# Kernel tuning notes

Measured on AMD Instinct MI355X. Metric: run time of the kernel, lower is better.

The kernel has to match this reference:

```python
import jax, jax.numpy as jnp
import numpy as np

N_NODES, N_EDGES, F_IN = 8192, 32768, 16
N_SUB, N_GRAPH = 512, 32
EDGE_DIM, HID = 5, 128
DIMS = [(16, 32), (32, 64), (64, 64)]  # (M_in, M_out) per NNConv layer


def _segment_mean(x, seg, n):
    s = jax.ops.segment_sum(x, seg, num_segments=n)
    c = jax.ops.segment_sum(jnp.ones((x.shape[0], 1), x.dtype), seg, num_segments=n)
    return s / jnp.maximum(c, 1.0)


def _nnconv(x, src, dst, eattr, W1, b1, W2, b2, root, bias):
    # edge MLP -> per-edge weight matrix theta: [E, M_in, M_out]
    h = jax.nn.relu(eattr @ W1 + b1)
    theta = (h @ W2 + b2).reshape(-1, x.shape[1], root.shape[1])
    msg = jnp.einsum('ei,eio->eo', x[src], theta)          # gather + per-edge matvec
    agg = jax.ops.segment_sum(msg, dst, num_segments=x.shape[0])  # scatter-add (aggr='add')
    return agg + x @ root + bias


def setup_inputs() -> dict:
    key = jax.random.key(0)
    ks = jax.random.split(key, 32)
    inp = {}
    inp['x'] = jax.random.normal(ks[0], (N_NODES, F_IN), jnp.float32)
    inp['edge_index'] = jax.random.randint(ks[1], (2, N_EDGES), 0, N_NODES)
    inp['edge_attr'] = jax.random.uniform(ks[2], (N_EDGES, EDGE_DIM), jnp.float32)
    inp['node_to_subgraph'] = jnp.sort(jax.random.randint(ks[3], (N_NODES,), 0, N_SUB))
    inp['subgraph_to_graph'] = jnp.sort(jax.random.randint(ks[4], (N_SUB,), 0, N_GRAPH))
    i = 5
    for l, (ci, co) in enumerate(DIMS):
        inp[f'W1_{l}'] = jax.random.normal(ks[i], (EDGE_DIM, HID), jnp.float32) * 0.1
        inp[f'b1_{l}'] = jnp.zeros((HID,), jnp.float32)
        inp[f'W2_{l}'] = jax.random.normal(ks[i + 1], (HID, ci * co), jnp.float32) * 0.05
        inp[f'b2_{l}'] = jnp.zeros((ci * co,), jnp.float32)
        inp[f'root_{l}'] = jax.random.normal(ks[i + 2], (ci, co), jnp.float32) * 0.1
        inp[f'bias_{l}'] = jnp.zeros((co,), jnp.float32)
        i += 3
    inp['fc1_w'] = jax.random.normal(ks[i], (64, 32), jnp.float32) * 0.1
    inp['fc1_b'] = jnp.zeros((32,), jnp.float32)
    inp['fc2_w'] = jax.random.normal(ks[i + 1], (32, 16), jnp.float32) * 0.1
    inp['fc2_b'] = jnp.zeros((16,), jnp.float32)
    inp['fc3_w'] = jax.random.normal(ks[i + 2], (16, 1), jnp.float32) * 0.1
    inp['fc3_b'] = jnp.zeros((1,), jnp.float32)
    return inp


def reference(x, edge_index, edge_attr, node_to_subgraph, subgraph_to_graph,
              W1_0, b1_0, W2_0, b2_0, root_0, bias_0,
              W1_1, b1_1, W2_1, b2_1, root_1, bias_1,
              W1_2, b1_2, W2_2, b2_2, root_2, bias_2,
              fc1_w, fc1_b, fc2_w, fc2_b, fc3_w, fc3_b):
    src, dst = edge_index[0], edge_index[1]
    layers = [(W1_0, b1_0, W2_0, b2_0, root_0, bias_0),
              (W1_1, b1_1, W2_1, b2_1, root_1, bias_1),
              (W1_2, b1_2, W2_2, b2_2, root_2, bias_2)]
    h = x
    for (W1, b1, W2, b2, root, bias) in layers:
        h = jax.nn.elu(_nnconv(h, src, dst, edge_attr, W1, b1, W2, b2, root, bias))
    h = _segment_mean(h, node_to_subgraph, N_SUB)      # global_mean_pool over subgraphs
    h = _segment_mean(h, subgraph_to_graph, N_GRAPH)   # global_mean_pool over graphs
    h = jax.nn.elu(h @ fc1_w + fc1_b)
    h = jax.nn.elu(h @ fc2_w + fc2_b)
    return (h @ fc3_w + fc3_b).reshape(-1)
```

## Files before the change

### kernel.cpp

```cpp
#include <hip/hip_runtime.h>

#define E_EDGES 32768
#define NN 8192
#define HID 128

typedef _Float16 half8 __attribute__((ext_vector_type(8)));
typedef _Float16 half4 __attribute__((ext_vector_type(4)));
typedef float f32x4 __attribute__((ext_vector_type(4)));

__device__ __forceinline__ void prep_one(int idx, int l2ci, int l2co,
                                         const float* __restrict__ W2,
                                         const float* __restrict__ b2,
                                         _Float16* __restrict__ out) {
  int CI = 1 << l2ci, CO = 1 << l2co;
  int Kmain = CI << 7;
  int j = idx & 7;
  int n = (idx >> 3) & (CO - 1);
  int kg = idx >> (3 + l2co);
  int k = kg * 8 + j;
  float v = 0.f;
  if (k < Kmain) {
    int hh = k >> l2ci, i = k & (CI - 1);
    v = W2[((hh << l2ci) + i) * CO + n];
  } else if (k < Kmain + CI) {
    v = b2[(k - Kmain) * CO + n];
  }
  out[idx] = (_Float16)v;
}

#define ZTOT (8192 * 32 + 8192 * 64 + 8192 * 64 + 512 * 64 + 512)
#define PREP0 (2176 * 32)
#define PREP1 (4224 * 64)
#define PREP2 (8320 * 64)

__global__ void prep_k(float* __restrict__ zr,
                       const float* __restrict__ W2a, const float* __restrict__ b2a, _Float16* __restrict__ oa,
                       const float* __restrict__ W2b, const float* __restrict__ b2b, _Float16* __restrict__ ob,
                       const float* __restrict__ W2c, const float* __restrict__ b2c, _Float16* __restrict__ oc) {
  int idx = blockIdx.x * 256 + threadIdx.x;
  if (idx < ZTOT) { zr[idx] = 0.f; return; }
  idx -= ZTOT;
  if (idx < PREP0) prep_one(idx, 4, 5, W2a, b2a, oa);
  else if (idx < PREP0 + PREP1) prep_one(idx - PREP0, 5, 6, W2b, b2b, ob);
  else if (idx < PREP0 + PREP1 + PREP2) prep_one(idx - PREP0 - PREP1, 6, 6, W2c, b2c, oc);
}

template <int CI, int CO>
__launch_bounds__(256, 2)
__global__ void msg_mfma_k(const float* __restrict__ xcur, const int* __restrict__ src,
                           const int* __restrict__ dst, const float* __restrict__ eattr,
                           const float* __restrict__ W1, const float* __restrict__ b1,
                           const _Float16* __restrict__ Bsw, float* __restrict__ agg) {
  constexpr int ME = 256;
  constexpr int L2CI = (CI == 64) ? 6 : ((CI == 32) ? 5 : 4);
  constexpr int XSTR = CI + 8;
  constexpr int FC = CO / 16;
  constexpr int C4 = CI / 4;
  constexpr int L2C4 = L2CI - 2;
  constexpr int NV = (CI == 64) ? 2 : 1;
  constexpr int HS = 40;
  constexpr int CW = CI / 4;
  constexpr int RR = CW / 4;

  __shared__ _Float16 he_t[ME * HS];
  __shared__ _Float16 xs_s[ME * XSTR];
  __shared__ float ea_s[ME * 5];
  __shared__ float W1s[5 * 32];
  __shared__ float b1s[32];
  __shared__ int src_s[ME];
  __shared__ int dst_s[ME];

  int t = threadIdx.x;
  int e0 = blockIdx.x * ME;
  int y = blockIdx.y;
  int hbeg = y * 32;

  for (int j = t; j < ME * 5; j += 256) ea_s[j] = eattr[e0 * 5 + j];
  if (t < 5 * 32) W1s[t] = W1[(t >> 5) * HID + hbeg + (t & 31)];
  if (t < 32) b1s[t] = b1[hbeg + t];
  src_s[t] = src[e0 + t];
  dst_s[t] = dst[e0 + t];
  __syncthreads();

  for (int j = t; j < 32 * ME; j += 256) {
    int hl = j >> 8, e = j & (ME - 1);
    float v = b1s[hl];
#pragma unroll
    for (int d = 0; d < 5; ++d) v += ea_s[e * 5 + d] * W1s[d * 32 + hl];
    he_t[e * HS + hl] = (_Float16)fmaxf(v, 0.f);
  }
  for (int j = t; j < ME * C4; j += 256) {
    int e = j >> L2C4, i4 = j & (C4 - 1);
    float4 v = ((const float4*)xcur)[src_s[e] * C4 + i4];
    half4 hq = {(_Float16)v.x, (_Float16)v.y, (_Float16)v.z, (_Float16)v.w};
    *(half4*)&xs_s[e * XSTR + i4 * 4] = hq;
  }
  __syncthreads();

  int lane = t & 63;
  int w = t >> 6;
  int quad = lane >> 4, l15 = lane & 15;

  half8 xreg[4][NV];
#pragma unroll
  for (int fr = 0; fr < 4; ++fr)
#pragma unroll
    for (int v = 0; v < NV; ++v)
      xreg[fr][v] = *(const half8*)&xs_s[(w * 64 + fr * 16 + l15) * XSTR +
                                         ((quad * 8 + v * 32) & (CI - 1))];

  int cbeg = y * CI;
  int ctail_end = cbeg + CI + ((y == 3) ? 4 : 0);

  const half8* bsw8 = (const half8*)Bsw;
  int ib = quad * CO + l15;

  f32x4 acc[4][FC];
#pragma unroll
  for (int fr = 0; fr < 4; ++fr)
#pragma unroll
    for (int fc = 0; fc < FC; ++fc)
#pragma unroll
      for (int r = 0; r < 4; ++r) acc[fr][fc][r] = 0.f;

  half8 breg[4][FC];
#pragma unroll
  for (int j = 0; j < 4; ++j)
#pragma unroll
    for (int fc = 0; fc < FC; ++fc)
      breg[j][fc] = bsw8[(cbeg + j) * 4 * CO + ib + fc * 16];

  for (int win = 0; win < 4; ++win) {
    half8 hreg[4];
#pragma unroll
    for (int fr = 0; fr < 4; ++fr)
      hreg[fr] = *(const half8*)&he_t[(w * 64 + fr * 16 + l15) * HS + win * 8];
#pragma unroll
    for (int rr = 0; rr < RR; ++rr) {
#pragma unroll
      for (int j = 0; j < 4; ++j) {
        int cl = win * CW + rr * 4 + j;
        int c = cbeg + cl;
        constexpr int PAR = (CI == 64) ? 1 : 0;
        int vi = PAR ? (cl & 1) : 0;
        half8 a[4];
#pragma unroll
        for (int fr = 0; fr < 4; ++fr) {
          _Float16 hv;
          if (CI == 16)      hv = (quad & 2) ? hreg[fr][2 * j + 1] : hreg[fr][2 * j];
          else if (CI == 32) hv = hreg[fr][rr * 4 + j];
          else               hv = hreg[fr][(rr * 4 + j) >> 1];
          half8 hb = {hv, hv, hv, hv, hv, hv, hv, hv};
          a[fr] = xreg[fr][vi] * hb;
        }
#pragma unroll
        for (int fc = 0; fc < FC; ++fc) {
#pragma unroll
          for (int fr = 0; fr < 4; ++fr)
            acc[fr][fc] = __builtin_amdgcn_mfma_f32_16x16x32_f16(a[fr], breg[cl & 3][fc], acc[fr][fc], 0, 0, 0);
        }
        int cn = c + 4;
        if (cn >= ctail_end) cn = ctail_end - 1;
#pragma unroll
        for (int fc = 0; fc < FC; ++fc)
          breg[cl & 3][fc] = bsw8[cn * 4 * CO + ib + fc * 16];
      }
    }
  }

  if (y == 3) {
#pragma unroll
    for (int j = 0; j < 4; ++j) {
      int cl = CI + j;
      constexpr int PAR = (CI == 64) ? 1 : 0;
      int vi = PAR ? (cl & 1) : 0;
#pragma unroll
      for (int fc = 0; fc < FC; ++fc) {
#pragma unroll
        for (int fr = 0; fr < 4; ++fr)
          acc[fr][fc] = __builtin_amdgcn_mfma_f32_16x16x32_f16(xreg[fr][vi], breg[cl & 3][fc], acc[fr][fc], 0, 0, 0);
      }
    }
  }

#pragma unroll
  for (int fr = 0; fr < 4; ++fr)
#pragma unroll
    for (int r = 0; r < 4; ++r) {
      int el = w * 64 + fr * 16 + quad * 4 + r;
      int d = dst_s[el];
      float* base = agg + (size_t)d * CO + l15;
#pragma unroll
      for (int fc = 0; fc < FC; ++fc)
        atomicAdd(base + fc * 16, acc[fr][fc][r]);
    }
}

template <int CI, int CO, bool POOL, bool CNT>
__global__ void fin_k(const float* __restrict__ xcur, const float* __restrict__ root,
                      const float* __restrict__ bias, const float* __restrict__ agg,
                      const int* __restrict__ n2s, int* __restrict__ cnt_sub,
                      float* __restrict__ ssum, float* __restrict__ xnext) {
  constexpr int NB = 256 / CO;
  __shared__ float xs[NB * CI];
  int t = threadIdx.x;
  int n0 = blockIdx.x * NB;
  for (int j = t; j < NB * CI; j += 256) xs[j] = xcur[n0 * CI + j];
  __syncthreads();
  int nl = t / CO, o = t & (CO - 1);
  int n = n0 + nl;
  float a = bias[o] + agg[n * CO + o];
#pragma unroll
  for (int i = 0; i < CI; ++i) a += xs[nl * CI + i] * root[i * CO + o];
  float r = a > 0.f ? a : expm1f(a);
  if (CNT && o == 0) atomicAdd(&cnt_sub[n2s[n]], 1);
  if (POOL) atomicAdd(&ssum[(n2s[n] << 6) + o], r);
  else xnext[n * CO + o] = r;
}

__device__ __forceinline__ int lbound(const int* __restrict__ a, int n, int v) {
  int lo = 0, hi = n;
  while (lo < hi) { int m = (lo + hi) >> 1; if (a[m] < v) lo = m + 1; else hi = m; }
  return lo;
}

__global__ void head_k(const float* __restrict__ ssum, const int* __restrict__ cnt_sub,
                       const int* __restrict__ s2g,
                       const float* __restrict__ w1, const float* __restrict__ b1,
                       const float* __restrict__ w2, const float* __restrict__ b2,
                       const float* __restrict__ w3, const float* __restrict__ b3,
                       float* __restrict__ out) {
  int g = blockIdx.x;
  int t = threadIdx.x;
  __shared__ float m[64], s1[32], s2[16];
  int slo = lbound(s2g, 512, g);
  int shi = lbound(s2g, 512, g + 1);
  float acc = 0.f;
  for (int s = slo; s < shi; ++s)
    acc += ssum[(s << 6) + t] / fmaxf((float)cnt_sub[s], 1.f);
  m[t] = acc / fmaxf((float)(shi - slo), 1.f);
  __syncthreads();
  if (t < 32) {
    float a = b1[t];
    for (int i = 0; i < 64; ++i) a += m[i] * w1[i * 32 + t];
    s1[t] = a > 0.f ? a : expm1f(a);
  }
  __syncthreads();
  if (t < 16) {
    float a = b2[t];
    for (int i = 0; i < 32; ++i) a += s1[i] * w2[i * 16 + t];
    s2[t] = a > 0.f ? a : expm1f(a);
  }
  __syncthreads();
  if (t == 0) {
    float a = b3[0];
    for (int i = 0; i < 16; ++i) a += s2[i] * w3[i];
    out[g] = a;
  }
}

extern "C" void kernel_launch(void* const* d_in, const int* in_sizes, int n_in,
                              void* d_out, int out_size, void* d_ws, size_t ws_size,
                              hipStream_t stream) {
  (void)in_sizes; (void)n_in; (void)out_size; (void)ws_size;
  const float* x0 = (const float*)d_in[0];
  const int* ei = (const int*)d_in[1];
  const float* ea = (const float*)d_in[2];
  const int* n2s = (const int*)d_in[3];
  const int* s2g = (const int*)d_in[4];
  const float* W1_[3] = {(const float*)d_in[5], (const float*)d_in[11], (const float*)d_in[17]};
  const float* b1_[3] = {(const float*)d_in[6], (const float*)d_in[12], (const float*)d_in[18]};
  const float* W2_[3] = {(const float*)d_in[7], (const float*)d_in[13], (const float*)d_in[19]};
  const float* b2_[3] = {(const float*)d_in[8], (const float*)d_in[14], (const float*)d_in[20]};
  const float* rt_[3] = {(const float*)d_in[9], (const float*)d_in[15], (const float*)d_in[21]};
  const float* bs_[3] = {(const float*)d_in[10], (const float*)d_in[16], (const float*)d_in[22]};
  const float* fc1w = (const float*)d_in[23]; const float* fc1b = (const float*)d_in[24];
  const float* fc2w = (const float*)d_in[25]; const float* fc2b = (const float*)d_in[26];
  const float* fc3w = (const float*)d_in[27]; const float* fc3b = (const float*)d_in[28];
  float* out = (float*)d_out;

  const int* srcp = ei;
  const int* dstp = ei + E_EDGES;

  char* wsb = (char*)d_ws;
  size_t off = 0;
  auto alloc = [&](size_t bytes) {
    void* p = wsb + off;
    off += (bytes + 255) & ~(size_t)255;
    return p;
  };
  _Float16* Bsw0 = (_Float16*)alloc((size_t)PREP0 * 2);
  _Float16* Bsw1 = (_Float16*)alloc((size_t)PREP1 * 2);
  _Float16* Bsw2 = (_Float16*)alloc((size_t)PREP2 * 2);
  float* agg1 = (float*)alloc((size_t)NN * 32 * 4);
  float* agg2 = (float*)alloc((size_t)NN * 64 * 4);
  float* agg3 = (float*)alloc((size_t)NN * 64 * 4);
  float* ssum = (float*)alloc((size_t)512 * 64 * 4);
  int* cnt_sub = (int*)alloc((size_t)512 * 4);
  float* x1 = (float*)alloc((size_t)NN * 32 * 4);
  float* x2 = (float*)alloc((size_t)NN * 64 * 4);

  const int preptot = ZTOT + PREP0 + PREP1 + PREP2;
  prep_k<<<(preptot + 255) / 256, 256, 0, stream>>>(agg1, W2_[0], b2_[0], Bsw0,
                                                    W2_[1], b2_[1], Bsw1,
                                                    W2_[2], b2_[2], Bsw2);

  dim3 mg(E_EDGES / 256, 4);
  msg_mfma_k<16, 32><<<mg, 256, 0, stream>>>(x0, srcp, dstp, ea, W1_[0], b1_[0], Bsw0, agg1);
  fin_k<16, 32, false, true><<<NN / 8, 256, 0, stream>>>(x0, rt_[0], bs_[0], agg1, n2s, cnt_sub, ssum, x1);
  msg_mfma_k<32, 64><<<mg, 256, 0, stream>>>(x1, srcp, dstp, ea, W1_[1], b1_[1], Bsw1, agg2);
  fin_k<32, 64, false, false><<<NN / 4, 256, 0, stream>>>(x1, rt_[1], bs_[1], agg2, n2s, cnt_sub, ssum, x2);
  msg_mfma_k<64, 64><<<mg, 256, 0, stream>>>(x2, srcp, dstp, ea, W1_[2], b1_[2], Bsw2, agg3);
  fin_k<64, 64, true, false><<<NN / 4, 256, 0, stream>>>(x2, rt_[2], bs_[2], agg3, n2s, cnt_sub, ssum, nullptr);

  head_k<<<32, 64, 0, stream>>>(ssum, cnt_sub, s2g, fc1w, fc1b, fc2w, fc2b, fc3w, fc3b, out);
}
```

Measured before the change: 282.6 us.

## Halve edge tile per block and shrink register buffers for higher occupancy

The edge tile per block drops from 256 to 128 edges, so each wave now handles 32 edges (2 fragments instead of 4). The B-operand register ring shrinks from 4 to 2 entries with a prefetch distance of 2, and launch bounds are raised to 4 blocks per CU. Together these cut register and LDS pressure and double the grid, aiming for better latency hiding and more parallelism. The cost is less reuse of each B load across edges (twice as many B global loads overall), a shorter prefetch distance, and a non-unrolled inner loop.

```diff
diff --git a/kernel.cpp b/kernel.cpp
--- a/kernel.cpp
+++ b/kernel.cpp
@@ -46,12 +46,12 @@
 }
 
 template <int CI, int CO>
-__launch_bounds__(256, 2)
+__launch_bounds__(256, 4)
 __global__ void msg_mfma_k(const float* __restrict__ xcur, const int* __restrict__ src,
                            const int* __restrict__ dst, const float* __restrict__ eattr,
                            const float* __restrict__ W1, const float* __restrict__ b1,
                            const _Float16* __restrict__ Bsw, float* __restrict__ agg) {
-  constexpr int ME = 256;
+  constexpr int ME = 128;
   constexpr int L2CI = (CI == 64) ? 6 : ((CI == 32) ? 5 : 4);
   constexpr int XSTR = CI + 8;
   constexpr int FC = CO / 16;
@@ -60,7 +60,7 @@
   constexpr int NV = (CI == 64) ? 2 : 1;
   constexpr int HS = 40;
   constexpr int CW = CI / 4;
-  constexpr int RR = CW / 4;
+  constexpr int NP = CW / 2;
 
   __shared__ _Float16 he_t[ME * HS];
   __shared__ _Float16 xs_s[ME * XSTR];
@@ -78,12 +78,11 @@
   for (int j = t; j < ME * 5; j += 256) ea_s[j] = eattr[e0 * 5 + j];
   if (t < 5 * 32) W1s[t] = W1[(t >> 5) * HID + hbeg + (t & 31)];
   if (t < 32) b1s[t] = b1[hbeg + t];
-  src_s[t] = src[e0 + t];
-  dst_s[t] = dst[e0 + t];
+  if (t < ME) { src_s[t] = src[e0 + t]; dst_s[t] = dst[e0 + t]; }
   __syncthreads();
 
   for (int j = t; j < 32 * ME; j += 256) {
-    int hl = j >> 8, e = j & (ME - 1);
+    int hl = j >> 7, e = j & (ME - 1);
     float v = b1s[hl];
 #pragma unroll
     for (int d = 0; d < 5; ++d) v += ea_s[e * 5 + d] * W1s[d * 32 + hl];
@@ -100,70 +99,68 @@
   int lane = t & 63;
   int w = t >> 6;
   int quad = lane >> 4, l15 = lane & 15;
-
-  half8 xreg[4][NV];
-#pragma unroll
-  for (int fr = 0; fr < 4; ++fr)
+  int hsel = (quad >> 1) & 1;
+
+  half8 xreg[2][NV];
+#pragma unroll
+  for (int fr = 0; fr < 2; ++fr)
 #pragma unroll
     for (int v = 0; v < NV; ++v)
-      xreg[fr][v] = *(const half8*)&xs_s[(w * 64 + fr * 16 + l15) * XSTR +
+      xreg[fr][v] = *(const half8*)&xs_s[(w * 32 + fr * 16 + l15) * XSTR +
                                          ((quad * 8 + v * 32) & (CI - 1))];
 
   int cbeg = y * CI;
-  int ctail_end = cbeg + CI + ((y == 3) ? 4 : 0);
+  int TC = CI + ((y == 3) ? 4 : 0);
 
   const half8* bsw8 = (const half8*)Bsw;
   int ib = quad * CO + l15;
 
-  f32x4 acc[4][FC];
-#pragma unroll
-  for (int fr = 0; fr < 4; ++fr)
+  f32x4 acc[2][FC];
+#pragma unroll
+  for (int fr = 0; fr < 2; ++fr)
 #pragma unroll
     for (int fc = 0; fc < FC; ++fc)
 #pragma unroll
       for (int r = 0; r < 4; ++r) acc[fr][fc][r] = 0.f;
 
-  half8 breg[4][FC];
-#pragma unroll
-  for (int j = 0; j < 4; ++j)
+  half8 breg[2][FC];
+#pragma unroll
+  for (int p = 0; p < 2; ++p)
 #pragma unroll
     for (int fc = 0; fc < FC; ++fc)
-      breg[j][fc] = bsw8[(cbeg + j) * 4 * CO + ib + fc * 16];
+      breg[p][fc] = bsw8[(cbeg + p) * 4 * CO + ib + fc * 16];
 
   for (int win = 0; win < 4; ++win) {
-    half8 hreg[4];
-#pragma unroll
-    for (int fr = 0; fr < 4; ++fr)
-      hreg[fr] = *(const half8*)&he_t[(w * 64 + fr * 16 + l15) * HS + win * 8];
-#pragma unroll
-    for (int rr = 0; rr < RR; ++rr) {
-#pragma unroll
-      for (int j = 0; j < 4; ++j) {
-        int cl = win * CW + rr * 4 + j;
-        int c = cbeg + cl;
-        constexpr int PAR = (CI == 64) ? 1 : 0;
-        int vi = PAR ? (cl & 1) : 0;
-        half8 a[4];
-#pragma unroll
-        for (int fr = 0; fr < 4; ++fr) {
+    half8 hreg[2];
+#pragma unroll
+    for (int fr = 0; fr < 2; ++fr)
+      hreg[fr] = *(const half8*)&he_t[(w * 32 + fr * 16 + l15) * HS + win * 8];
+    for (int cl2 = 0; cl2 < NP; ++cl2) {
+#pragma unroll
+      for (int p = 0; p < 2; ++p) {
+        int cl = win * CW + cl2 * 2 + p;
+        int vi = (CI == 64) ? p : 0;
+        half8 a[2];
+#pragma unroll
+        for (int fr = 0; fr < 2; ++fr) {
           _Float16 hv;
-          if (CI == 16)      hv = (quad & 2) ? hreg[fr][2 * j + 1] : hreg[fr][2 * j];
-          else if (CI == 32) hv = hreg[fr][rr * 4 + j];
-          else               hv = hreg[fr][(rr * 4 + j) >> 1];
+          if (CI == 16)      hv = hreg[fr][2 * (cl2 * 2 + p) + hsel];
+          else if (CI == 32) hv = hreg[fr][cl2 * 2 + p];
+          else               hv = hreg[fr][cl2];
           half8 hb = {hv, hv, hv, hv, hv, hv, hv, hv};
           a[fr] = xreg[fr][vi] * hb;
         }
 #pragma unroll
         for (int fc = 0; fc < FC; ++fc) {
 #pragma unroll
-          for (int fr = 0; fr < 4; ++fr)
-            acc[fr][fc] = __builtin_amdgcn_mfma_f32_16x16x32_f16(a[fr], breg[cl & 3][fc], acc[fr][fc], 0, 0, 0);
+          for (int fr = 0; fr < 2; ++fr)
+            acc[fr][fc] = __builtin_amdgcn_mfma_f32_16x16x32_f16(a[fr], breg[p][fc], acc[fr][fc], 0, 0, 0);
         }
-        int cn = c + 4;
-        if (cn >= ctail_end) cn = ctail_end - 1;
+        int cn = cl + 2;
+        if (cn >= TC) cn = TC - 1;
 #pragma unroll
         for (int fc = 0; fc < FC; ++fc)
-          breg[cl & 3][fc] = bsw8[cn * 4 * CO + ib + fc * 16];
+          breg[p][fc] = bsw8[(cbeg + cn) * 4 * CO + ib + fc * 16];
       }
     }
   }
@@ -172,22 +169,27 @@
 #pragma unroll
     for (int j = 0; j < 4; ++j) {
       int cl = CI + j;
-      constexpr int PAR = (CI == 64) ? 1 : 0;
-      int vi = PAR ? (cl & 1) : 0;
+      int p = j & 1;
+      int vi = (CI == 64) ? p : 0;
 #pragma unroll
       for (int fc = 0; fc < FC; ++fc) {
 #pragma unroll
-        for (int fr = 0; fr < 4; ++fr)
-          acc[fr][fc] = __builtin_amdgcn_mfma_f32_16x16x32_f16(xreg[fr][vi], breg[cl & 3][fc], acc[fr][fc], 0, 0, 0);
+        for (int fr = 0; fr < 2; ++fr)
+          acc[fr][fc] = __builtin_amdgcn_mfma_f32_16x16x32_f16(xreg[fr][vi], breg[p][fc], acc[fr][fc], 0, 0, 0);
       }
+      int cn = cl + 2;
+      if (cn >= TC) cn = TC - 1;
+#pragma unroll
+      for (int fc = 0; fc < FC; ++fc)
+        breg[p][fc] = bsw8[(cbeg + cn) * 4 * CO + ib + fc * 16];
     }
   }
 
 #pragma unroll
-  for (int fr = 0; fr < 4; ++fr)
+  for (int fr = 0; fr < 2; ++fr)
 #pragma unroll
     for (int r = 0; r < 4; ++r) {
-      int el = w * 64 + fr * 16 + quad * 4 + r;
+      int el = w * 32 + fr * 16 + quad * 4 + r;
       int d = dst_s[el];
       float* base = agg + (size_t)d * CO + l15;
 #pragma unroll
@@ -305,7 +307,7 @@
                                                     W2_[1], b2_[1], Bsw1,
                                                     W2_[2], b2_[2], Bsw2);
 
-  dim3 mg(E_EDGES / 256, 4);
+  dim3 mg(E_EDGES / 128, 4);
   msg_mfma_k<16, 32><<<mg, 256, 0, stream>>>(x0, srcp, dstp, ea, W1_[0], b1_[0], Bsw0, agg1);
   fin_k<16, 32, false, true><<<NN / 8, 256, 0, stream>>>(x0, rt_[0], bs_[0], agg1, n2s, cnt_sub, ssum, x1);
   msg_mfma_k<32, 64><<<mg, 256, 0, stream>>>(x1, srcp, dstp, ea, W1_[1], b1_[1], Bsw1, agg2);
```

Result: no change. 281.6 us (-0.3%).
